# Kernel tuning notes

Hardware: AMD Instinct MI355X
Metric: run time of the kernel (lower is better)

Reference implementation:

```python
import jax, jax.numpy as jnp
import numpy as np

B, K, F, E = 32, 1024, 128, 128  # batch, window_size(num_nodes), n_features, embed_dim
OUT2 = 125                       # lin2 output dim (hardcoded in module)
ALPHA = 0.2                      # LeakyReLU negative slope


def setup_inputs() -> dict:
    key = jax.random.key(0)
    ks = jax.random.split(key, 7)
    x = jax.random.normal(ks[0], (B, K, F), dtype=jnp.float32)
    lin_w = jax.random.normal(ks[1], (E, F), dtype=jnp.float32) * 0.05
    lin_b = jax.random.normal(ks[2], (E,), dtype=jnp.float32) * 0.01
    a = jax.random.normal(ks[3], (2 * E, 1), dtype=jnp.float32) * 0.1  # xavier-ish
    bias = jax.random.normal(ks[4], (K, K), dtype=jnp.float32) * 0.02
    lin2_w = jax.random.normal(ks[5], (OUT2, K), dtype=jnp.float32) * 0.03
    lin2_b = jax.random.normal(ks[6], (OUT2,), dtype=jnp.float32) * 0.01
    return {"x": x, "lin_w": lin_w, "lin_b": lin_b, "a": a, "bias": bias,
            "lin2_w": lin2_w, "lin2_b": lin2_b}


def reference(x, lin_w, lin_b, a, bias, lin2_w, lin2_b):
    # Wx = lin(x): [B,K,E]
    Wx = jnp.einsum('bkf,ef->bke', x, lin_w) + lin_b
    # Additive attention scores. Original concatenates (Wx_i, Wx_j) -> [B,K,K,2E]
    # then matmuls with a [2E,1]. Identity: concat @ a == Wx_i@a1 + Wx_j@a2.
    a1 = a[:E, 0]   # [E]
    a2 = a[E:, 0]   # [E]
    s1 = Wx @ a1    # [B,K]  (row/query term, from repeat_interleave)
    s2 = Wx @ a2    # [B,K]  (col/key term, from repeat)
    e = jax.nn.leaky_relu(s1[:, :, None] + s2[:, None, :], negative_slope=ALPHA)
    e = e + bias                              # [B,K,K]
    attention = jax.nn.softmax(e, axis=2)     # softmax over last dim (keys)
    h = jnp.einsum('bij,bjf->bif', attention, x) + x   # [B,K,F], residual
    # permute(0,2,1) -> [B,F,K]; lin2 contracts K -> 125
    h2 = jnp.einsum('bkf,ok->bfo', h, lin2_w) + lin2_b  # [B,F,125]
    h2 = jax.nn.relu(h2)
    return (h2, attention)
```

## Files before the change

kernel.cpp:

```cpp
#include <hip/hip_runtime.h>

#define B_ 32
#define K_ 1024
#define F_ 128
#define E_ 128
#define OUT2_ 125
#define ALPHA_ 0.2f

typedef __bf16 bf16x8_t __attribute__((ext_vector_type(8)));
typedef float  f32x4_t  __attribute__((ext_vector_type(4)));

__global__ void k_prep(const float* __restrict__ lin_w, const float* __restrict__ lin_b,
                       const float* __restrict__ a, float* __restrict__ ws) {
    int t = threadIdx.x;
    if (t < 128) {
        float acc = 0.f;
        for (int e = 0; e < E_; ++e) acc += lin_w[e * F_ + t] * a[e];
        ws[t] = acc;
    } else {
        int f = t - 128;
        float acc = 0.f;
        for (int e = 0; e < E_; ++e) acc += lin_w[e * F_ + f] * a[E_ + e];
        ws[128 + f] = acc;
    }
    if (t == 0) { float c = 0.f; for (int e = 0; e < E_; ++e) c += lin_b[e] * a[e];       ws[256] = c; }
    if (t == 1) { float c = 0.f; for (int e = 0; e < E_; ++e) c += lin_b[e] * a[E_ + e];  ws[257] = c; }
}

__global__ __launch_bounds__(256) void k_xts(const float* __restrict__ x,
                                             const float* __restrict__ ws,
                                             unsigned short* __restrict__ xt,
                                             float* __restrict__ s1,
                                             float* __restrict__ s2) {
    int kt = blockIdx.x;
    int b  = blockIdx.y;
    int t  = threadIdx.x;
    __shared__ float xs[64 * 132];
    __shared__ float red1[4][64], red2[4][64];
    const float* xb = x + ((size_t)b * K_ + kt * 64) * F_;
#pragma unroll
    for (int q = 0; q < 8; ++q) {
        int flat = q * 256 + t;
        int kk = flat >> 5, f4 = flat & 31;
        float4 v = *(const float4*)(xb + (size_t)kk * F_ + f4 * 4);
        xs[kk * 132 + f4 * 4]     = v.x;
        xs[kk * 132 + f4 * 4 + 1] = v.y;
        xs[kk * 132 + f4 * 4 + 2] = v.z;
        xs[kk * 132 + f4 * 4 + 3] = v.w;
    }
    __syncthreads();
    {
        int f = t >> 1, half = t & 1;
        union { __bf16 h[32]; uint4 v[4]; } pack;
#pragma unroll
        for (int i = 0; i < 32; ++i) pack.h[i] = (__bf16)xs[(half * 32 + i) * 132 + f];
        unsigned short* dst = xt + (((size_t)(b * 16 + kt) * 128 + f) * 64 + half * 32);
        uint4* d4 = (uint4*)dst;
#pragma unroll
        for (int i = 0; i < 4; ++i) d4[i] = pack.v[i];
    }
    {
        int r = t & 63, p = t >> 6;
        const float4* xr = (const float4*)&xs[r * 132 + p * 32];
        const float4* w1 = (const float4*)&ws[p * 32];
        const float4* w2 = (const float4*)&ws[128 + p * 32];
        float a1 = 0.f, a2 = 0.f;
#pragma unroll
        for (int q = 0; q < 8; ++q) {
            float4 xv = xr[q];
            float4 wa = w1[q], wb = w2[q];
            a1 += xv.x * wa.x + xv.y * wa.y + xv.z * wa.z + xv.w * wa.w;
            a2 += xv.x * wb.x + xv.y * wb.y + xv.z * wb.z + xv.w * wb.w;
        }
        red1[p][r] = a1; red2[p][r] = a2;
    }
    __syncthreads();
    if (t < 64) {
        s1[(size_t)b * K_ + kt * 64 + t] =
            red1[0][t] + red1[1][t] + red1[2][t] + red1[3][t] + ws[256];
    } else if (t < 128) {
        int r = t - 64;
        s2[(size_t)b * K_ + kt * 64 + r] =
            red2[0][r] + red2[1][r] + red2[2][r] + red2[3][r] + ws[257];
    }
}

__global__ __launch_bounds__(256) void k_softmax(const float* __restrict__ s1,
                                                 const float* __restrict__ s2,
                                                 const float* __restrict__ bias,
                                                 float* __restrict__ att) {
    int i = blockIdx.x >> 5;
    int b = blockIdx.x & 31;
    int t = threadIdx.x;
    float sv = s1[b * K_ + i];
    float4 s2v = ((const float4*)(s2 + b * K_))[t];
    float4 bv  = ((const float4*)(bias + (size_t)i * K_))[t];
    float e[4];
    {
        float v;
        v = sv + s2v.x; v = v > 0.f ? v : ALPHA_ * v; e[0] = __expf(v + bv.x);
        v = sv + s2v.y; v = v > 0.f ? v : ALPHA_ * v; e[1] = __expf(v + bv.y);
        v = sv + s2v.z; v = v > 0.f ? v : ALPHA_ * v; e[2] = __expf(v + bv.z);
        v = sv + s2v.w; v = v > 0.f ? v : ALPHA_ * v; e[3] = __expf(v + bv.w);
    }
    float sum = e[0] + e[1] + e[2] + e[3];
    for (int m = 32; m; m >>= 1) sum += __shfl_xor(sum, m, 64);
    __shared__ float reds[4];
    int wave = t >> 6, lane = t & 63;
    if (lane == 0) reds[wave] = sum;
    __syncthreads();
    sum = reds[0] + reds[1] + reds[2] + reds[3];
    float r = 1.f / sum;
    float4 o; o.x = e[0] * r; o.y = e[1] * r; o.z = e[2] * r; o.w = e[3] * r;
    ((float4*)(att + ((size_t)b * K_ + i) * K_))[t] = o;
}

__global__ __launch_bounds__(256, 4) void k_attx(const float* __restrict__ att,
                                                 const unsigned short* __restrict__ xt,
                                                 const float* __restrict__ x,
                                                 unsigned short* __restrict__ ht) {
    int b  = blockIdx.y;
    int i0 = blockIdx.x * 32;
    int t  = threadIdx.x;
    int wave = t >> 6, lane = t & 63;
    int quad = lane >> 4, l15 = lane & 15;

    __shared__ unsigned short X_s[2][128 * 64];

    const float* ab  = att + ((size_t)b * K_ + i0) * K_;
    const uint4* xtb = (const uint4*)(xt + (size_t)b * 16 * 128 * 64);

    f32x4_t acc[2][2];
#pragma unroll
    for (int m = 0; m < 2; ++m)
#pragma unroll
        for (int n = 0; n < 2; ++n) acc[m][n] = (f32x4_t)(0.f);

#pragma unroll
    for (int q = 0; q < 4; ++q) {
        int flat = q * 256 + t;
        int row = flat >> 3, g = flat & 7;
        *(uint4*)&X_s[0][row * 64 + 8 * (g ^ (row & 7))] = xtb[flat];
    }
    __syncthreads();

    int cur = 0;
    for (int kt = 0; kt < 16; ++kt) {
        int k0 = kt * 64;
        uint4 xn[4];
        if (kt < 15) {
            const uint4* src = xtb + (size_t)(kt + 1) * 1024;
#pragma unroll
            for (int q = 0; q < 4; ++q) xn[q] = src[q * 256 + t];
        }
        float4 av[2][2][2];
#pragma unroll
        for (int m = 0; m < 2; ++m) {
            const float* arow = ab + (size_t)(m * 16 + l15) * K_ + k0 + quad * 8;
#pragma unroll
            for (int kh = 0; kh < 2; ++kh) {
                av[m][kh][0] = *(const float4*)(arow + kh * 32);
                av[m][kh][1] = *(const float4*)(arow + kh * 32 + 4);
            }
        }
#pragma unroll
        for (int kh = 0; kh < 2; ++kh) {
            bf16x8_t af[2], bff[2];
#pragma unroll
            for (int m = 0; m < 2; ++m) {
                union { __bf16 h[8]; bf16x8_t v; } p;
                float4 v0 = av[m][kh][0], v1 = av[m][kh][1];
                p.h[0] = (__bf16)v0.x; p.h[1] = (__bf16)v0.y;
                p.h[2] = (__bf16)v0.z; p.h[3] = (__bf16)v0.w;
                p.h[4] = (__bf16)v1.x; p.h[5] = (__bf16)v1.y;
                p.h[6] = (__bf16)v1.z; p.h[7] = (__bf16)v1.w;
                af[m] = p.v;
            }
#pragma unroll
            for (int n = 0; n < 2; ++n) {
                int row = wave * 32 + n * 16 + l15;
                bff[n] = *(const bf16x8_t*)&X_s[cur][row * 64 + 8 * (((kh << 2) | quad) ^ (row & 7))];
            }
#pragma unroll
            for (int m = 0; m < 2; ++m)
#pragma unroll
                for (int n = 0; n < 2; ++n)
                    acc[m][n] = __builtin_amdgcn_mfma_f32_16x16x32_bf16(af[m], bff[n], acc[m][n], 0, 0, 0);
        }
        if (kt < 15) {
#pragma unroll
            for (int q = 0; q < 4; ++q) {
                int flat = q * 256 + t;
                int row = flat >> 3, g = flat & 7;
                *(uint4*)&X_s[cur ^ 1][row * 64 + 8 * (g ^ (row & 7))] = xn[q];
            }
        }
        __syncthreads();
        cur ^= 1;
    }
#pragma unroll
    for (int m = 0; m < 2; ++m) {
#pragma unroll
        for (int n = 0; n < 2; ++n) {
            int f = wave * 32 + n * 16 + l15;
            int ib = i0 + m * 16 + quad * 4;
            union { __bf16 h[4]; ushort4 v; } p;
#pragma unroll
            for (int r = 0; r < 4; ++r) {
                int i = ib + r;
                p.h[r] = (__bf16)(acc[m][n][r] + x[((size_t)b * K_ + i) * F_ + f]);
            }
            *(ushort4*)&ht[((size_t)b * F_ + f) * K_ + ib] = p.v;
        }
    }
}

__global__ __launch_bounds__(256) void k_out2m(const unsigned short* __restrict__ ht,
                                               const float* __restrict__ w2,
                                               float* __restrict__ part) {
    int b  = blockIdx.y;
    int f0 = blockIdx.x * 64;
    int ks = blockIdx.z;
    int t  = threadIdx.x;
    int wave = t >> 6, lane = t & 63;
    int quad = lane >> 4, l15 = lane & 15;

    __shared__ unsigned short W_s[128 * 72];
    __shared__ unsigned short H_s[64 * 72];

    f32x4_t acc[8];
#pragma unroll
    for (int m = 0; m < 8; ++m) acc[m] = (f32x4_t)(0.f);

    int wo = t >> 1, wq = t & 1;
    int hf = t >> 2, hq = t & 3;

    int kt0 = ks * 4;
    for (int kt = kt0; kt < kt0 + 4; ++kt) {
        int k0 = kt * 64;
        __syncthreads();
        {
            union { __bf16 h[32]; uint4 v[4]; } p;
            if (wo < OUT2_) {
                const float* src = w2 + (size_t)wo * K_ + k0 + wq * 32;
#pragma unroll
                for (int q = 0; q < 8; ++q) {
                    float4 v = *(const float4*)(src + q * 4);
                    p.h[q * 4]     = (__bf16)v.x;
                    p.h[q * 4 + 1] = (__bf16)v.y;
                    p.h[q * 4 + 2] = (__bf16)v.z;
                    p.h[q * 4 + 3] = (__bf16)v.w;
                }
            } else {
#pragma unroll
                for (int q = 0; q < 4; ++q) p.v[q] = make_uint4(0, 0, 0, 0);
            }
            uint4* d = (uint4*)&W_s[wo * 72 + wq * 32];
#pragma unroll
            for (int q = 0; q < 4; ++q) d[q] = p.v[q];
        }
        {
            const uint4* src = (const uint4*)(ht + ((size_t)b * F_ + f0 + hf) * K_ + k0) + hq * 2;
            uint4* d = (uint4*)&H_s[hf * 72 + hq * 16];
            d[0] = src[0]; d[1] = src[1];
        }
        __syncthreads();
#pragma unroll
        for (int kh = 0; kh < 2; ++kh) {
            bf16x8_t bf = *(const bf16x8_t*)&H_s[(wave * 16 + l15) * 72 + kh * 32 + quad * 8];
#pragma unroll
            for (int m = 0; m < 8; ++m) {
                bf16x8_t af = *(const bf16x8_t*)&W_s[(m * 16 + l15) * 72 + kh * 32 + quad * 8];
                acc[m] = __builtin_amdgcn_mfma_f32_16x16x32_bf16(af, bf, acc[m], 0, 0, 0);
            }
        }
    }
    int f = f0 + wave * 16 + l15;
    float* prow = part + ((size_t)(ks * 32 + b) * 128 + f) * 128;
#pragma unroll
    for (int m = 0; m < 8; ++m)
        *(f32x4_t*)&prow[m * 16 + quad * 4] = acc[m];
}

__global__ __launch_bounds__(256) void k_out2e(const float* __restrict__ part,
                                               const float* __restrict__ b2,
                                               float* __restrict__ out) {
    int idx = blockIdx.x * 256 + threadIdx.x;
    if (idx >= B_ * F_ * OUT2_) return;
    int o  = idx % OUT2_;
    int bf = idx / OUT2_;
    float v = b2[o];
#pragma unroll
    for (int s = 0; s < 4; ++s) v += part[((size_t)s * 4096 + bf) * 128 + o];
    out[idx] = v > 0.f ? v : 0.f;
}

extern "C" void kernel_launch(void* const* d_in, const int* in_sizes, int n_in,
                              void* d_out, int out_size, void* d_ws, size_t ws_size,
                              hipStream_t stream) {
    const float* x      = (const float*)d_in[0];
    const float* lin_w  = (const float*)d_in[1];
    const float* lin_b  = (const float*)d_in[2];
    const float* a      = (const float*)d_in[3];
    const float* bias   = (const float*)d_in[4];
    const float* lin2_w = (const float*)d_in[5];
    const float* lin2_b = (const float*)d_in[6];

    float* out = (float*)d_out;
    float* h2  = out;
    float* att = out + (size_t)B_ * F_ * OUT2_;

    float* ws = (float*)d_ws;
    float* s1 = ws + 512;
    float* s2 = ws + 512 + B_ * K_;
    unsigned short* ht = (unsigned short*)(ws + 512 + 2 * B_ * K_);
    unsigned short* xt = ht + (size_t)B_ * K_ * F_;
    float* part = (float*)xt;

    k_prep<<<1, 256, 0, stream>>>(lin_w, lin_b, a, ws);
    k_xts<<<dim3(16, B_), 256, 0, stream>>>(x, ws, xt, s1, s2);
    k_softmax<<<B_ * K_, 256, 0, stream>>>(s1, s2, bias, att);
    k_attx<<<dim3(K_ / 32, B_), 256, 0, stream>>>(att, xt, x, ht);
    k_out2m<<<dim3(2, B_, 4), 256, 0, stream>>>(ht, lin2_w, part);
    k_out2e<<<(B_ * F_ * OUT2_ + 255) / 256, 256, 0, stream>>>(part, lin2_b, h2);
}
```

Baseline: 283.6 us.

## Fuse prep into xts kernel and register-prefetch attention tiles in attx

Drops the single-block k_prep launch. Each k_xts block now computes the lin_w·a projection vectors itself, redundantly, into shared memory, which removes one launch and a serial dependency. In k_attx the fp32 attention rows for the next k-tile are loaded into registers one iteration ahead and converted to bf16 after the MFMAs, so global load latency overlaps compute. The loop is also fully unrolled. The costs are redundant prep work in each of the 512 blocks and higher register pressure under launch_bounds(256,4).

```diff
diff --git a/kernel.cpp b/kernel.cpp
--- a/kernel.cpp
+++ b/kernel.cpp
@@ -10,25 +10,10 @@
 typedef __bf16 bf16x8_t __attribute__((ext_vector_type(8)));
 typedef float  f32x4_t  __attribute__((ext_vector_type(4)));
 
-__global__ void k_prep(const float* __restrict__ lin_w, const float* __restrict__ lin_b,
-                       const float* __restrict__ a, float* __restrict__ ws) {
-    int t = threadIdx.x;
-    if (t < 128) {
-        float acc = 0.f;
-        for (int e = 0; e < E_; ++e) acc += lin_w[e * F_ + t] * a[e];
-        ws[t] = acc;
-    } else {
-        int f = t - 128;
-        float acc = 0.f;
-        for (int e = 0; e < E_; ++e) acc += lin_w[e * F_ + f] * a[E_ + e];
-        ws[128 + f] = acc;
-    }
-    if (t == 0) { float c = 0.f; for (int e = 0; e < E_; ++e) c += lin_b[e] * a[e];       ws[256] = c; }
-    if (t == 1) { float c = 0.f; for (int e = 0; e < E_; ++e) c += lin_b[e] * a[E_ + e];  ws[257] = c; }
-}
-
 __global__ __launch_bounds__(256) void k_xts(const float* __restrict__ x,
-                                             const float* __restrict__ ws,
+                                             const float* __restrict__ lin_w,
+                                             const float* __restrict__ lin_b,
+                                             const float* __restrict__ a,
                                              unsigned short* __restrict__ xt,
                                              float* __restrict__ s1,
                                              float* __restrict__ s2) {
@@ -37,6 +22,23 @@
     int t  = threadIdx.x;
     __shared__ float xs[64 * 132];
     __shared__ float red1[4][64], red2[4][64];
+    __shared__ float wsl[260];
+
+    {
+        int f = t & 127, sel = t >> 7;
+        const float* av = a + sel * 128;
+        float acc = 0.f;
+#pragma unroll 8
+        for (int e = 0; e < E_; ++e) acc += lin_w[e * F_ + f] * av[e];
+        wsl[sel * 128 + f] = acc;
+        if (t < 2) {
+            const float* aw = a + t * 128;
+            float c = 0.f;
+#pragma unroll 8
+            for (int e = 0; e < E_; ++e) c += lin_b[e] * aw[e];
+            wsl[256 + t] = c;
+        }
+    }
     const float* xb = x + ((size_t)b * K_ + kt * 64) * F_;
 #pragma unroll
     for (int q = 0; q < 8; ++q) {
@@ -62,8 +64,8 @@
     {
         int r = t & 63, p = t >> 6;
         const float4* xr = (const float4*)&xs[r * 132 + p * 32];
-        const float4* w1 = (const float4*)&ws[p * 32];
-        const float4* w2 = (const float4*)&ws[128 + p * 32];
+        const float4* w1 = (const float4*)&wsl[p * 32];
+        const float4* w2 = (const float4*)&wsl[128 + p * 32];
         float a1 = 0.f, a2 = 0.f;
 #pragma unroll
         for (int q = 0; q < 8; ++q) {
@@ -77,11 +79,11 @@
     __syncthreads();
     if (t < 64) {
         s1[(size_t)b * K_ + kt * 64 + t] =
-            red1[0][t] + red1[1][t] + red1[2][t] + red1[3][t] + ws[256];
+            red1[0][t] + red1[1][t] + red1[2][t] + red1[3][t] + wsl[256];
     } else if (t < 128) {
         int r = t - 64;
         s2[(size_t)b * K_ + kt * 64 + r] =
-            red2[0][r] + red2[1][r] + red2[2][r] + red2[3][r] + ws[257];
+            red2[0][r] + red2[1][r] + red2[2][r] + red2[3][r] + wsl[257];
     }
 }
 
@@ -130,52 +132,68 @@
     const float* ab  = att + ((size_t)b * K_ + i0) * K_;
     const uint4* xtb = (const uint4*)(xt + (size_t)b * 16 * 128 * 64);
 
+    const float* arow[2];
+    arow[0] = ab + (size_t)l15 * K_ + quad * 8;
+    arow[1] = arow[0] + 16 * K_;
+
     f32x4_t acc[2][2];
 #pragma unroll
     for (int m = 0; m < 2; ++m)
 #pragma unroll
         for (int n = 0; n < 2; ++n) acc[m][n] = (f32x4_t)(0.f);
 
-#pragma unroll
-    for (int q = 0; q < 4; ++q) {
-        int flat = q * 256 + t;
-        int row = flat >> 3, g = flat & 7;
-        *(uint4*)&X_s[0][row * 64 + 8 * (g ^ (row & 7))] = xtb[flat];
-    }
-    __syncthreads();
-
-    int cur = 0;
-    for (int kt = 0; kt < 16; ++kt) {
-        int k0 = kt * 64;
-        uint4 xn[4];
-        if (kt < 15) {
-            const uint4* src = xtb + (size_t)(kt + 1) * 1024;
-#pragma unroll
-            for (int q = 0; q < 4; ++q) xn[q] = src[q * 256 + t];
-        }
+    bf16x8_t afc[2][2];
+    {
         float4 av[2][2][2];
 #pragma unroll
-        for (int m = 0; m < 2; ++m) {
-            const float* arow = ab + (size_t)(m * 16 + l15) * K_ + k0 + quad * 8;
+        for (int m = 0; m < 2; ++m)
 #pragma unroll
             for (int kh = 0; kh < 2; ++kh) {
-                av[m][kh][0] = *(const float4*)(arow + kh * 32);
-                av[m][kh][1] = *(const float4*)(arow + kh * 32 + 4);
-            }
-        }
-#pragma unroll
-        for (int kh = 0; kh < 2; ++kh) {
-            bf16x8_t af[2], bff[2];
-#pragma unroll
-            for (int m = 0; m < 2; ++m) {
+                av[m][kh][0] = *(const float4*)(arow[m] + kh * 32);
+                av[m][kh][1] = *(const float4*)(arow[m] + kh * 32 + 4);
+            }
+#pragma unroll
+        for (int q = 0; q < 4; ++q) {
+            int flat = q * 256 + t;
+            int row = flat >> 3, g = flat & 7;
+            *(uint4*)&X_s[0][row * 64 + 8 * (g ^ (row & 7))] = xtb[flat];
+        }
+#pragma unroll
+        for (int m = 0; m < 2; ++m)
+#pragma unroll
+            for (int kh = 0; kh < 2; ++kh) {
                 union { __bf16 h[8]; bf16x8_t v; } p;
                 float4 v0 = av[m][kh][0], v1 = av[m][kh][1];
                 p.h[0] = (__bf16)v0.x; p.h[1] = (__bf16)v0.y;
                 p.h[2] = (__bf16)v0.z; p.h[3] = (__bf16)v0.w;
                 p.h[4] = (__bf16)v1.x; p.h[5] = (__bf16)v1.y;
                 p.h[6] = (__bf16)v1.z; p.h[7] = (__bf16)v1.w;
-                af[m] = p.v;
-            }
+                afc[m][kh] = p.v;
+            }
+    }
+    __syncthreads();
+
+    int cur = 0;
+#pragma unroll
+    for (int kt = 0; kt < 16; ++kt) {
+        uint4 xn[4];
+        float4 av[2][2][2];
+        if (kt < 15) {
+            const uint4* src = xtb + (size_t)(kt + 1) * 1024;
+#pragma unroll
+            for (int q = 0; q < 4; ++q) xn[q] = src[q * 256 + t];
+            int ko = (kt + 1) * 64;
+#pragma unroll
+            for (int m = 0; m < 2; ++m)
+#pragma unroll
+                for (int kh = 0; kh < 2; ++kh) {
+                    av[m][kh][0] = *(const float4*)(arow[m] + ko + kh * 32);
+                    av[m][kh][1] = *(const float4*)(arow[m] + ko + kh * 32 + 4);
+                }
+        }
+#pragma unroll
+        for (int kh = 0; kh < 2; ++kh) {
+            bf16x8_t bff[2];
 #pragma unroll
             for (int n = 0; n < 2; ++n) {
                 int row = wave * 32 + n * 16 + l15;
@@ -185,9 +203,21 @@
             for (int m = 0; m < 2; ++m)
 #pragma unroll
                 for (int n = 0; n < 2; ++n)
-                    acc[m][n] = __builtin_amdgcn_mfma_f32_16x16x32_bf16(af[m], bff[n], acc[m][n], 0, 0, 0);
+                    acc[m][n] = __builtin_amdgcn_mfma_f32_16x16x32_bf16(afc[m][kh], bff[n], acc[m][n], 0, 0, 0);
         }
         if (kt < 15) {
+#pragma unroll
+            for (int m = 0; m < 2; ++m)
+#pragma unroll
+                for (int kh = 0; kh < 2; ++kh) {
+                    union { __bf16 h[8]; bf16x8_t v; } p;
+                    float4 v0 = av[m][kh][0], v1 = av[m][kh][1];
+                    p.h[0] = (__bf16)v0.x; p.h[1] = (__bf16)v0.y;
+                    p.h[2] = (__bf16)v0.z; p.h[3] = (__bf16)v0.w;
+                    p.h[4] = (__bf16)v1.x; p.h[5] = (__bf16)v1.y;
+                    p.h[6] = (__bf16)v1.z; p.h[7] = (__bf16)v1.w;
+                    afc[m][kh] = p.v;
+                }
 #pragma unroll
             for (int q = 0; q < 4; ++q) {
                 int flat = q * 256 + t;
@@ -317,8 +347,7 @@
     unsigned short* xt = ht + (size_t)B_ * K_ * F_;
     float* part = (float*)xt;
 
-    k_prep<<<1, 256, 0, stream>>>(lin_w, lin_b, a, ws);
-    k_xts<<<dim3(16, B_), 256, 0, stream>>>(x, ws, xt, s1, s2);
+    k_xts<<<dim3(16, B_), 256, 0, stream>>>(x, lin_w, lin_b, a, xt, s1, s2);
     k_softmax<<<B_ * K_, 256, 0, stream>>>(s1, s2, bias, att);
     k_attx<<<dim3(K_ / 32, B_), 256, 0, stream>>>(att, xt, x, ht);
     k_out2m<<<dim3(2, B_, 4), 256, 0, stream>>>(ht, lin2_w, part);
```

Result: no change. 280.1 us (-1.2%).
